# Kernel tuning notes

Measured on AMD Instinct MI355X. Metric: run time of the kernel, lower is better.

The kernel has to match this reference:

```python
import jax, jax.numpy as jnp
import numpy as np

T, M, D_IN, N = 4096, 512, 11, 51


def setup_inputs() -> dict:
    key = jax.random.key(0)
    ks = jax.random.split(key, 11)
    s = 1.0 / np.sqrt(N)  # torch LSTMCell/Linear default init scale
    return {
        "input": jax.random.normal(ks[0], (T, M, D_IN), dtype=jnp.float32),
        "W_ih1": jax.random.uniform(ks[1], (4 * N, D_IN), jnp.float32, -s, s),
        "W_hh1": jax.random.uniform(ks[2], (4 * N, N), jnp.float32, -s, s),
        "b_ih1": jax.random.uniform(ks[3], (4 * N,), jnp.float32, -s, s),
        "b_hh1": jax.random.uniform(ks[4], (4 * N,), jnp.float32, -s, s),
        "W_ih2": jax.random.uniform(ks[5], (4 * N, N), jnp.float32, -s, s),
        "W_hh2": jax.random.uniform(ks[6], (4 * N, N), jnp.float32, -s, s),
        "b_ih2": jax.random.uniform(ks[7], (4 * N,), jnp.float32, -s, s),
        "b_hh2": jax.random.uniform(ks[8], (4 * N,), jnp.float32, -s, s),
        "W_lin": jax.random.uniform(ks[9], (1, N), jnp.float32, -s, s),
        "b_lin": jax.random.uniform(ks[10], (1,), jnp.float32, -s, s),
        "future": 0,
    }


def _lstm_cell(x, h, c, W_ih, W_hh, b_ih, b_hh):
    # torch gate order: input, forget, cell(g), output
    gates = x @ W_ih.T + b_ih + h @ W_hh.T + b_hh  # [m, 4n]
    i, f, g, o = jnp.split(gates, 4, axis=-1)
    c_new = jax.nn.sigmoid(f) * c + jax.nn.sigmoid(i) * jnp.tanh(g)
    h_new = jax.nn.sigmoid(o) * jnp.tanh(c_new)
    return h_new, c_new


def reference(input, W_ih1, W_hh1, b_ih1, b_hh1, W_ih2, W_hh2, b_ih2, b_hh2,
              W_lin, b_lin, future):
    m = input.shape[1]
    n = W_hh1.shape[1]
    h1 = jnp.zeros((m, n), jnp.float32)
    c1 = jnp.zeros((m, n), jnp.float32)
    h2 = jnp.zeros((m, n), jnp.float32)
    c2 = jnp.zeros((m, n), jnp.float32)

    def step(carry, x_t):
        h1, c1, h2, c2 = carry
        h1, c1 = _lstm_cell(x_t, h1, c1, W_ih1, W_hh1, b_ih1, b_hh1)
        h2, c2 = _lstm_cell(h1, h2, c2, W_ih2, W_hh2, b_ih2, b_hh2)
        out = h2 @ W_lin.T + b_lin  # [m, 1]
        return (h1, c1, h2, c2), out

    _, outs = jax.lax.scan(step, (h1, c1, h2, c2), input)  # [T, m, 1]
    # torch.stack(outputs, 1).squeeze(2) -> [m, T]
    # (future loop is dimensionally invalid in the original for future>0; future=0)
    return outs[:, :, 0].T
```

## Files before the change

kernel.cpp:

```cpp
#include <hip/hip_runtime.h>

#define T_STEPS 4096
#define M_BATCH 512
#define D_INP   11
#define N_HID   51
#define L1S     76
#define L2S     140

typedef __attribute__((ext_vector_type(8))) short bf16x8;
typedef __attribute__((ext_vector_type(4))) float f32x4;
typedef __attribute__((ext_vector_type(4))) short s16x4;

__device__ __forceinline__ float sigmoid_fast(float v) {
    return __builtin_amdgcn_rcpf(1.0f + __expf(-v));
}
__device__ __forceinline__ float tanh_fast(float v) {
    return 2.0f * __builtin_amdgcn_rcpf(1.0f + __expf(-2.0f * v)) - 1.0f;
}
__device__ __forceinline__ ushort f2bf(float f) {
    uint u = __float_as_uint(f);
    u += 0x7fffu + ((u >> 16) & 1u);
    return (ushort)(u >> 16);
}
__device__ __forceinline__ float bf2f(ushort h) {
    return __uint_as_float(((uint)h) << 16);
}

#define MFMA(A,B,C) __builtin_amdgcn_mfma_f32_16x16x32_bf16((A),(B),(C),0,0,0)

__attribute__((amdgpu_waves_per_eu(2, 2)))
__global__ __launch_bounds__(512)
void lstm2_mfma8(const float* __restrict__ input,
                 const float* __restrict__ W_ih1, const float* __restrict__ W_hh1,
                 const float* __restrict__ b_ih1, const float* __restrict__ b_hh1,
                 const float* __restrict__ W_ih2, const float* __restrict__ W_hh2,
                 const float* __restrict__ b_ih2, const float* __restrict__ b_hh2,
                 const float* __restrict__ W_lin, const float* __restrict__ b_lin,
                 float* __restrict__ out)
{
    const int tid  = threadIdx.x;
    const int wid  = tid >> 6;
    const int lane = tid & 63;
    const int mr   = lane & 15;
    const int g    = lane >> 4;
    const int col0 = blockIdx.x * 16;
    const bool isL1 = wid < 3;
    const int  m0   = isL1 ? ((wid == 0) ? 0 : (wid == 1) ? 5 : 10)
                           : (wid - 3) * 3;

    __shared__ __align__(16) ushort l1act[16][L1S];
    __shared__ __align__(16) ushort l2act[16][L2S];
    __shared__ __align__(16) ushort xck[2][16][16][12];
    __shared__ __align__(16) float  outb[16][64];

    for (int i = tid; i < 16 * L1S; i += 512) (&l1act[0][0])[i] = 0;
    for (int i = tid; i < 16 * L2S; i += 512) (&l2act[0][0])[i] = 0;
    for (int i = tid; i < 2 * 16 * 16 * 12; i += 512) (&xck[0][0][0][0])[i] = 0;
    for (int i = tid; i < 16 * 64; i += 512) (&outb[0][0])[i] = 0.f;

    float xr[6];
    auto xissue = [&](int cn) {
        #pragma unroll
        for (int i = 0; i < 6; ++i) {
            int f = i * 512 + tid;
            if (f < 2816) {
                int s = f / 176, r2 = f - s * 176;
                int cc = r2 / 11, d = r2 - cc * 11;
                int ts = cn * 16 + s; if (ts > T_STEPS - 1) ts = T_STEPS - 1;
                xr[i] = input[((size_t)ts * M_BATCH + col0 + cc) * D_INP + d];
            }
        }
    };
    auto xwrite = [&](int cn) {
        #pragma unroll
        for (int i = 0; i < 6; ++i) {
            int f = i * 512 + tid;
            if (f < 2816) {
                int s = f / 176, r2 = f - s * 176;
                int cc = r2 / 11, d = r2 - cc * 11;
                xck[cn & 1][s][cc][d] = f2bf(xr[i]);
            }
        }
    };

    auto wgetL1 = [&](int r, int k) -> float {
        if (r >= 204) return 0.f;
        int u = r >> 2, q = r & 3;
        if (k < 12) return (k < 11) ? W_ih1[(q * 51 + u) * 11 + k] : 0.f;
        int hu = k - 12; return (hu < 51) ? W_hh1[(q * 51 + u) * 51 + hu] : 0.f;
    };
    auto wgetL2 = [&](int r, int k) -> float {
        if (r == 204) return (k >= 51 && k < 102) ? W_lin[k - 51] : 0.f;
        if (r > 204) return 0.f;
        int u = r >> 2, q = r & 3;
        if (k < 51)  return W_ih2[(q * 51 + u) * 51 + k];
        if (k < 102) return W_hh2[(q * 51 + u) * 51 + (k - 51)];
        return 0.f;
    };
    auto mkfragL1 = [&](int m, int kt, int ver) -> bf16x8 {
        bf16x8 fr;
        #pragma unroll
        for (int j = 0; j < 8; ++j) {
            int k = 32 * kt + 16 * (j >> 2) + 4 * g + (j & 3);
            float w = wgetL1(16 * m + mr, k);
            ushort hi = f2bf(w);
            fr[j] = (short)((ver == 0) ? hi : f2bf(w - bf2f(hi)));
        }
        return fr;
    };
    auto mkfragL2 = [&](int m, int kt, int ver) -> bf16x8 {
        bf16x8 fr;
        #pragma unroll
        for (int j = 0; j < 8; ++j) {
            int k = 32 * kt + 16 * (j >> 2) + 4 * g + (j & 3);
            float w = wgetL2(16 * m + mr, k);
            ushort hi = f2bf(w);
            fr[j] = (short)((ver == 0) ? hi : f2bf(w - bf2f(hi)));
        }
        return fr;
    };

    bf16x8 afr[24];
    if (wid < 2) {
        #pragma unroll
        for (int mt = 0; mt < 5; ++mt)
            #pragma unroll
            for (int kt = 0; kt < 2; ++kt)
                #pragma unroll
                for (int v = 0; v < 2; ++v)
                    afr[(mt * 2 + kt) * 2 + v] = mkfragL1(m0 + mt, kt, v);
    } else if (wid == 2) {
        #pragma unroll
        for (int mt = 0; mt < 3; ++mt)
            #pragma unroll
            for (int kt = 0; kt < 2; ++kt)
                #pragma unroll
                for (int v = 0; v < 2; ++v)
                    afr[(mt * 2 + kt) * 2 + v] = mkfragL1(m0 + mt, kt, v);
    } else if (wid < 7) {
        #pragma unroll
        for (int mt = 0; mt < 3; ++mt)
            #pragma unroll
            for (int kt = 0; kt < 4; ++kt)
                #pragma unroll
                for (int v = 0; v < 2; ++v)
                    afr[(mt * 4 + kt) * 2 + v] = mkfragL2(m0 + mt, kt, v);
    } else {
        #pragma unroll
        for (int kt = 0; kt < 4; ++kt)
            #pragma unroll
            for (int v = 0; v < 2; ++v)
                afr[kt * 2 + v] = mkfragL2(12, kt, v);
    }

    f32x4 br[5];
    #pragma unroll
    for (int mt = 0; mt < 5; ++mt) {
        int u = 4 * (m0 + mt) + g;
        f32x4 b = {0.f, 0.f, 0.f, 0.f};
        if (u < N_HID) {
            #pragma unroll
            for (int q = 0; q < 4; ++q)
                b[q] = isL1 ? (b_ih1[q * 51 + u] + b_hh1[q * 51 + u])
                            : (b_ih2[q * 51 + u] + b_hh2[q * 51 + u]);
        } else if (!isL1 && u == N_HID) {
            b[0] = b_lin[0];
        }
        br[mt] = b;
    }

    f32x4 acc[5];
    float cst[5];
    #pragma unroll
    for (int i = 0; i < 5; ++i) cst[i] = 0.f;

    auto lstm = [&](f32x4 gg, float& cs) -> float {
        float iv = sigmoid_fast(gg.x), fv = sigmoid_fast(gg.y);
        float gv = tanh_fast(gg.z),    ov = sigmoid_fast(gg.w);
        cs = fv * cs + iv * gv;
        return ov * tanh_fast(cs);
    };

    xissue(0); xwrite(0);
    __syncthreads();

    #pragma unroll 1
    for (int t = 0; t <= T_STEPS + 1; ++t) {
        const int xb = (t >> 4) & 1, xs = t & 15;

        if ((t & 15) == 2 && t <= T_STEPS - 14) xissue((t >> 4) + 1);

        auto loadB1 = [&](int kt) -> bf16x8 {
            int k0 = 32 * kt + 4 * g;
            const ushort* pa = (k0 < 12) ? &xck[xb][xs][mr][k0] : &l1act[mr][k0 - 12];
            s16x4 va = *(const s16x4*)pa;
            s16x4 vb = *(const s16x4*)&l1act[mr][k0 + 4];
            bf16x8 r;
            r[0]=va[0]; r[1]=va[1]; r[2]=va[2]; r[3]=va[3];
            r[4]=vb[0]; r[5]=vb[1]; r[6]=vb[2]; r[7]=vb[3];
            return r;
        };
        auto loadB2 = [&](int kt) -> bf16x8 {
            int k0 = 32 * kt + 4 * g;
            s16x4 va = *(const s16x4*)&l2act[mr][k0];
            s16x4 vb = *(const s16x4*)&l2act[mr][k0 + 16];
            bf16x8 r;
            r[0]=va[0]; r[1]=va[1]; r[2]=va[2]; r[3]=va[3];
            r[4]=vb[0]; r[5]=vb[1]; r[6]=vb[2]; r[7]=vb[3];
            return r;
        };

        if (isL1) {
            bf16x8 b0 = loadB1(0), b1 = loadB1(1);
            if (wid < 2) {
                #pragma unroll
                for (int mt = 0; mt < 5; ++mt) {
                    f32x4 aH = {0.f,0.f,0.f,0.f}, aL = {0.f,0.f,0.f,0.f};
                    aH = MFMA(afr[(mt*2+0)*2+0], b0, aH);
                    aH = MFMA(afr[(mt*2+1)*2+0], b1, aH);
                    aL = MFMA(afr[(mt*2+0)*2+1], b0, aL);
                    aL = MFMA(afr[(mt*2+1)*2+1], b1, aL);
                    acc[mt] = aH + aL;
                }
            } else {
                #pragma unroll
                for (int mt = 0; mt < 3; ++mt) {
                    f32x4 aH = {0.f,0.f,0.f,0.f}, aL = {0.f,0.f,0.f,0.f};
                    aH = MFMA(afr[(mt*2+0)*2+0], b0, aH);
                    aH = MFMA(afr[(mt*2+1)*2+0], b1, aH);
                    aL = MFMA(afr[(mt*2+0)*2+1], b0, aL);
                    aL = MFMA(afr[(mt*2+1)*2+1], b1, aL);
                    acc[mt] = aH + aL;
                }
            }
        } else {
            bf16x8 c0 = loadB2(0), c1 = loadB2(1), c2 = loadB2(2), c3 = loadB2(3);
            if (wid < 7) {
                #pragma unroll
                for (int mt = 0; mt < 3; ++mt) {
                    f32x4 aH = {0.f,0.f,0.f,0.f}, aL = {0.f,0.f,0.f,0.f};
                    aH = MFMA(afr[(mt*4+0)*2+0], c0, aH);
                    aH = MFMA(afr[(mt*4+1)*2+0], c1, aH);
                    aH = MFMA(afr[(mt*4+2)*2+0], c2, aH);
                    aH = MFMA(afr[(mt*4+3)*2+0], c3, aH);
                    aL = MFMA(afr[(mt*4+0)*2+1], c0, aL);
                    aL = MFMA(afr[(mt*4+1)*2+1], c1, aL);
                    aL = MFMA(afr[(mt*4+2)*2+1], c2, aL);
                    aL = MFMA(afr[(mt*4+3)*2+1], c3, aL);
                    acc[mt] = aH + aL;
                }
            } else {
                f32x4 aH = {0.f,0.f,0.f,0.f}, aL = {0.f,0.f,0.f,0.f};
                aH = MFMA(afr[0*2+0], c0, aH);
                aH = MFMA(afr[1*2+0], c1, aH);
                aH = MFMA(afr[2*2+0], c2, aH);
                aH = MFMA(afr[3*2+0], c3, aH);
                aL = MFMA(afr[0*2+1], c0, aL);
                aL = MFMA(afr[1*2+1], c1, aL);
                aL = MFMA(afr[2*2+1], c2, aL);
                aL = MFMA(afr[3*2+1], c3, aL);
                acc[0] = aH + aL;
            }
        }
        __syncthreads();

        if (wid < 2) {
            #pragma unroll
            for (int mt = 0; mt < 5; ++mt) {
                f32x4 gg = acc[mt] + br[mt];
                float h = lstm(gg, cst[mt]);
                int u = 4 * (m0 + mt) + g;
                ushort hb = f2bf(h);
                l1act[mr][u] = hb; l2act[mr][u] = hb;
            }
        } else if (wid == 2) {
            #pragma unroll
            for (int mt = 0; mt < 3; ++mt) {
                f32x4 gg = acc[mt] + br[mt];
                float h = lstm(gg, cst[mt]);
                int u = 4 * (10 + mt) + g;
                if (u < N_HID) { ushort hb = f2bf(h); l1act[mr][u] = hb; l2act[mr][u] = hb; }
            }
        } else if (wid < 7) {
            if (t >= 1) {
                #pragma unroll
                for (int mt = 0; mt < 3; ++mt) {
                    f32x4 gg = acc[mt] + br[mt];
                    float h = lstm(gg, cst[mt]);
                    int u = 4 * (m0 + mt) + g;
                    l2act[mr][N_HID + u] = f2bf(h);
                }
            }
        } else {
            f32x4 gg = acc[0] + br[0];
            if (g == 3) {
                if (t >= 2) outb[mr][(t - 2) & 63] = gg.x;
            } else if (t >= 1) {
                float h = lstm(gg, cst[0]);
                l2act[mr][N_HID + 48 + g] = f2bf(h);
            }
        }

        if ((t & 15) == 10 && t <= T_STEPS - 6) xwrite((t >> 4) + 1);

        if ((t & 31) == 2 && t >= 34) {
            int tb0 = t - 34, cc = tid >> 5, j = tid & 31;
            out[(size_t)(col0 + cc) * T_STEPS + tb0 + j] = outb[cc][(tb0 + j) & 63];
        }
        __syncthreads();
    }

    {
        int tb0 = 4064, cc = tid >> 5, j = tid & 31;
        out[(size_t)(col0 + cc) * T_STEPS + tb0 + j] = outb[cc][(tb0 + j) & 63];
    }
}

extern "C" void kernel_launch(void* const* d_in, const int* in_sizes, int n_in,
                              void* d_out, int out_size, void* d_ws, size_t ws_size,
                              hipStream_t stream) {
    const float* input = (const float*)d_in[0];
    const float* W_ih1 = (const float*)d_in[1];
    const float* W_hh1 = (const float*)d_in[2];
    const float* b_ih1 = (const float*)d_in[3];
    const float* b_hh1 = (const float*)d_in[4];
    const float* W_ih2 = (const float*)d_in[5];
    const float* W_hh2 = (const float*)d_in[6];
    const float* b_ih2 = (const float*)d_in[7];
    const float* b_hh2 = (const float*)d_in[8];
    const float* W_lin = (const float*)d_in[9];
    const float* b_lin = (const float*)d_in[10];
    float* out = (float*)d_out;

    lstm2_mfma8<<<M_BATCH / 16, 512, 0, stream>>>(
        input, W_ih1, W_hh1, b_ih1, b_hh1,
        W_ih2, W_hh2, b_ih2, b_hh2, W_lin, b_lin, out);
}
```

Measured before the change: 5.058 ms.

## Spread LSTM gate tiles over 16 waves with double-buffered activations

Doubles the workgroup to 1024 threads (16 waves, 8 per layer) so each wave handles at most two 16-row gate tiles instead of up to five, shortening the per-step critical path. Hidden-state buffers are merged and double-buffered by timestep parity, which removes the mid-step barrier so only one __syncthreads per step remains. The linear-output wave is folded into the last layer-2 wave. The cost is more waves competing for the CU, fewer registers per wave, and a heavier block-wide barrier.

```diff
diff --git a/kernel.cpp b/kernel.cpp
--- a/kernel.cpp
+++ b/kernel.cpp
@@ -4,8 +4,7 @@
 #define M_BATCH 512
 #define D_INP   11
 #define N_HID   51
-#define L1S     76
-#define L2S     140
+#define ACTS    140
 
 typedef __attribute__((ext_vector_type(8))) short bf16x8;
 typedef __attribute__((ext_vector_type(4))) float f32x4;
@@ -28,15 +27,15 @@
 
 #define MFMA(A,B,C) __builtin_amdgcn_mfma_f32_16x16x32_bf16((A),(B),(C),0,0,0)
 
-__attribute__((amdgpu_waves_per_eu(2, 2)))
-__global__ __launch_bounds__(512)
-void lstm2_mfma8(const float* __restrict__ input,
-                 const float* __restrict__ W_ih1, const float* __restrict__ W_hh1,
-                 const float* __restrict__ b_ih1, const float* __restrict__ b_hh1,
-                 const float* __restrict__ W_ih2, const float* __restrict__ W_hh2,
-                 const float* __restrict__ b_ih2, const float* __restrict__ b_hh2,
-                 const float* __restrict__ W_lin, const float* __restrict__ b_lin,
-                 float* __restrict__ out)
+__attribute__((amdgpu_waves_per_eu(4, 4)))
+__global__ __launch_bounds__(1024)
+void lstm2_mfma16(const float* __restrict__ input,
+                  const float* __restrict__ W_ih1, const float* __restrict__ W_hh1,
+                  const float* __restrict__ b_ih1, const float* __restrict__ b_hh1,
+                  const float* __restrict__ W_ih2, const float* __restrict__ W_hh2,
+                  const float* __restrict__ b_ih2, const float* __restrict__ b_hh2,
+                  const float* __restrict__ W_lin, const float* __restrict__ b_lin,
+                  float* __restrict__ out)
 {
     const int tid  = threadIdx.x;
     const int wid  = tid >> 6;
@@ -44,25 +43,23 @@
     const int mr   = lane & 15;
     const int g    = lane >> 4;
     const int col0 = blockIdx.x * 16;
-    const bool isL1 = wid < 3;
-    const int  m0   = isL1 ? ((wid == 0) ? 0 : (wid == 1) ? 5 : 10)
-                           : (wid - 3) * 3;
-
-    __shared__ __align__(16) ushort l1act[16][L1S];
-    __shared__ __align__(16) ushort l2act[16][L2S];
+    const bool isL1 = wid < 8;
+    const int  lw   = isL1 ? wid : wid - 8;
+    const int  m0   = (lw < 5) ? lw * 2 : 10 + (lw - 5);
+
+    __shared__ __align__(16) ushort act[2][16][ACTS];
     __shared__ __align__(16) ushort xck[2][16][16][12];
     __shared__ __align__(16) float  outb[16][64];
 
-    for (int i = tid; i < 16 * L1S; i += 512) (&l1act[0][0])[i] = 0;
-    for (int i = tid; i < 16 * L2S; i += 512) (&l2act[0][0])[i] = 0;
-    for (int i = tid; i < 2 * 16 * 16 * 12; i += 512) (&xck[0][0][0][0])[i] = 0;
-    for (int i = tid; i < 16 * 64; i += 512) (&outb[0][0])[i] = 0.f;
-
-    float xr[6];
+    for (int i = tid; i < 2 * 16 * ACTS; i += 1024) (&act[0][0][0])[i] = 0;
+    for (int i = tid; i < 2 * 16 * 16 * 12; i += 1024) (&xck[0][0][0][0])[i] = 0;
+    for (int i = tid; i < 16 * 64; i += 1024) (&outb[0][0])[i] = 0.f;
+
+    float xr[3];
     auto xissue = [&](int cn) {
         #pragma unroll
-        for (int i = 0; i < 6; ++i) {
-            int f = i * 512 + tid;
+        for (int i = 0; i < 3; ++i) {
+            int f = i * 1024 + tid;
             if (f < 2816) {
                 int s = f / 176, r2 = f - s * 176;
                 int cc = r2 / 11, d = r2 - cc * 11;
@@ -73,8 +70,8 @@
     };
     auto xwrite = [&](int cn) {
         #pragma unroll
-        for (int i = 0; i < 6; ++i) {
-            int f = i * 512 + tid;
+        for (int i = 0; i < 3; ++i) {
+            int f = i * 1024 + tid;
             if (f < 2816) {
                 int s = f / 176, r2 = f - s * 176;
                 int cc = r2 / 11, d = r2 - cc * 11;
@@ -120,42 +117,44 @@
         return fr;
     };
 
-    bf16x8 afr[24];
-    if (wid < 2) {
-        #pragma unroll
-        for (int mt = 0; mt < 5; ++mt)
+    bf16x8 afr[16];
+    if (isL1) {
+        if (lw < 5) {
+            #pragma unroll
+            for (int mt = 0; mt < 2; ++mt)
+                #pragma unroll
+                for (int kt = 0; kt < 2; ++kt)
+                    #pragma unroll
+                    for (int v = 0; v < 2; ++v)
+                        afr[(mt * 2 + kt) * 2 + v] = mkfragL1(m0 + mt, kt, v);
+        } else {
             #pragma unroll
             for (int kt = 0; kt < 2; ++kt)
                 #pragma unroll
                 for (int v = 0; v < 2; ++v)
-                    afr[(mt * 2 + kt) * 2 + v] = mkfragL1(m0 + mt, kt, v);
-    } else if (wid == 2) {
-        #pragma unroll
-        for (int mt = 0; mt < 3; ++mt)
-            #pragma unroll
-            for (int kt = 0; kt < 2; ++kt)
+                    afr[kt * 2 + v] = mkfragL1(m0, kt, v);
+        }
+    } else {
+        if (lw < 5) {
+            #pragma unroll
+            for (int mt = 0; mt < 2; ++mt)
+                #pragma unroll
+                for (int kt = 0; kt < 4; ++kt)
+                    #pragma unroll
+                    for (int v = 0; v < 2; ++v)
+                        afr[(mt * 4 + kt) * 2 + v] = mkfragL2(m0 + mt, kt, v);
+        } else {
+            #pragma unroll
+            for (int kt = 0; kt < 4; ++kt)
                 #pragma unroll
                 for (int v = 0; v < 2; ++v)
-                    afr[(mt * 2 + kt) * 2 + v] = mkfragL1(m0 + mt, kt, v);
-    } else if (wid < 7) {
-        #pragma unroll
-        for (int mt = 0; mt < 3; ++mt)
-            #pragma unroll
-            for (int kt = 0; kt < 4; ++kt)
-                #pragma unroll
-                for (int v = 0; v < 2; ++v)
-                    afr[(mt * 4 + kt) * 2 + v] = mkfragL2(m0 + mt, kt, v);
-    } else {
-        #pragma unroll
-        for (int kt = 0; kt < 4; ++kt)
-            #pragma unroll
-            for (int v = 0; v < 2; ++v)
-                afr[kt * 2 + v] = mkfragL2(12, kt, v);
+                    afr[kt * 2 + v] = mkfragL2(m0, kt, v);
+        }
     }
 
-    f32x4 br[5];
+    f32x4 br[2];
     #pragma unroll
-    for (int mt = 0; mt < 5; ++mt) {
+    for (int mt = 0; mt < 2; ++mt) {
         int u = 4 * (m0 + mt) + g;
         f32x4 b = {0.f, 0.f, 0.f, 0.f};
         if (u < N_HID) {
@@ -169,10 +168,8 @@
         br[mt] = b;
     }
 
-    f32x4 acc[5];
-    float cst[5];
-    #pragma unroll
-    for (int i = 0; i < 5; ++i) cst[i] = 0.f;
+    f32x4 acc[2];
+    float cst[2] = {0.f, 0.f};
 
     auto lstm = [&](f32x4 gg, float& cs) -> float {
         float iv = sigmoid_fast(gg.x), fv = sigmoid_fast(gg.y);
@@ -181,20 +178,23 @@
         return ov * tanh_fast(cs);
     };
 
-    xissue(0); xwrite(0);
+    xissue(0);
+    __syncthreads();
+    xwrite(0);
     __syncthreads();
 
     #pragma unroll 1
     for (int t = 0; t <= T_STEPS + 1; ++t) {
-        const int xb = (t >> 4) & 1, xs = t & 15;
+        const int p = t & 1, q = p ^ 1;
+        const int xb = (t >> 4) & 1, xst = t & 15;
 
         if ((t & 15) == 2 && t <= T_STEPS - 14) xissue((t >> 4) + 1);
 
         auto loadB1 = [&](int kt) -> bf16x8 {
             int k0 = 32 * kt + 4 * g;
-            const ushort* pa = (k0 < 12) ? &xck[xb][xs][mr][k0] : &l1act[mr][k0 - 12];
+            const ushort* pa = (k0 < 12) ? &xck[xb][xst][mr][k0] : &act[p][mr][k0 - 12];
             s16x4 va = *(const s16x4*)pa;
-            s16x4 vb = *(const s16x4*)&l1act[mr][k0 + 4];
+            s16x4 vb = *(const s16x4*)&act[p][mr][k0 + 4];
             bf16x8 r;
             r[0]=va[0]; r[1]=va[1]; r[2]=va[2]; r[3]=va[3];
             r[4]=vb[0]; r[5]=vb[1]; r[6]=vb[2]; r[7]=vb[3];
@@ -202,8 +202,8 @@
         };
         auto loadB2 = [&](int kt) -> bf16x8 {
             int k0 = 32 * kt + 4 * g;
-            s16x4 va = *(const s16x4*)&l2act[mr][k0];
-            s16x4 vb = *(const s16x4*)&l2act[mr][k0 + 16];
+            s16x4 va = *(const s16x4*)&act[p][mr][k0];
+            s16x4 vb = *(const s16x4*)&act[p][mr][k0 + 16];
             bf16x8 r;
             r[0]=va[0]; r[1]=va[1]; r[2]=va[2]; r[3]=va[3];
             r[4]=vb[0]; r[5]=vb[1]; r[6]=vb[2]; r[7]=vb[3];
@@ -212,9 +212,9 @@
 
         if (isL1) {
             bf16x8 b0 = loadB1(0), b1 = loadB1(1);
-            if (wid < 2) {
-                #pragma unroll
-                for (int mt = 0; mt < 5; ++mt) {
+            if (lw < 5) {
+                #pragma unroll
+                for (int mt = 0; mt < 2; ++mt) {
                     f32x4 aH = {0.f,0.f,0.f,0.f}, aL = {0.f,0.f,0.f,0.f};
                     aH = MFMA(afr[(mt*2+0)*2+0], b0, aH);
                     aH = MFMA(afr[(mt*2+1)*2+0], b1, aH);
@@ -223,21 +223,18 @@
                     acc[mt] = aH + aL;
                 }
             } else {
-                #pragma unroll
-                for (int mt = 0; mt < 3; ++mt) {
-                    f32x4 aH = {0.f,0.f,0.f,0.f}, aL = {0.f,0.f,0.f,0.f};
-                    aH = MFMA(afr[(mt*2+0)*2+0], b0, aH);
-                    aH = MFMA(afr[(mt*2+1)*2+0], b1, aH);
-                    aL = MFMA(afr[(mt*2+0)*2+1], b0, aL);
-                    aL = MFMA(afr[(mt*2+1)*2+1], b1, aL);
-                    acc[mt] = aH + aL;
-                }
+                f32x4 aH = {0.f,0.f,0.f,0.f}, aL = {0.f,0.f,0.f,0.f};
+                aH = MFMA(afr[0*2+0], b0, aH);
+                aH = MFMA(afr[1*2+0], b1, aH);
+                aL = MFMA(afr[0*2+1], b0, aL);
+                aL = MFMA(afr[1*2+1], b1, aL);
+                acc[0] = aH + aL;
             }
         } else {
             bf16x8 c0 = loadB2(0), c1 = loadB2(1), c2 = loadB2(2), c3 = loadB2(3);
-            if (wid < 7) {
-                #pragma unroll
-                for (int mt = 0; mt < 3; ++mt) {
+            if (lw < 5) {
+                #pragma unroll
+                for (int mt = 0; mt < 2; ++mt) {
                     f32x4 aH = {0.f,0.f,0.f,0.f}, aL = {0.f,0.f,0.f,0.f};
                     aH = MFMA(afr[(mt*4+0)*2+0], c0, aH);
                     aH = MFMA(afr[(mt*4+1)*2+0], c1, aH);
@@ -262,57 +259,57 @@
                 acc[0] = aH + aL;
             }
         }
-        __syncthreads();
-
-        if (wid < 2) {
-            #pragma unroll
-            for (int mt = 0; mt < 5; ++mt) {
-                f32x4 gg = acc[mt] + br[mt];
-                float h = lstm(gg, cst[mt]);
-                int u = 4 * (m0 + mt) + g;
-                ushort hb = f2bf(h);
-                l1act[mr][u] = hb; l2act[mr][u] = hb;
-            }
-        } else if (wid == 2) {
-            #pragma unroll
-            for (int mt = 0; mt < 3; ++mt) {
-                f32x4 gg = acc[mt] + br[mt];
-                float h = lstm(gg, cst[mt]);
-                int u = 4 * (10 + mt) + g;
-                if (u < N_HID) { ushort hb = f2bf(h); l1act[mr][u] = hb; l2act[mr][u] = hb; }
-            }
-        } else if (wid < 7) {
-            if (t >= 1) {
-                #pragma unroll
-                for (int mt = 0; mt < 3; ++mt) {
+
+        if (isL1) {
+            if (lw < 5) {
+                #pragma unroll
+                for (int mt = 0; mt < 2; ++mt) {
                     f32x4 gg = acc[mt] + br[mt];
                     float h = lstm(gg, cst[mt]);
-                    int u = 4 * (m0 + mt) + g;
-                    l2act[mr][N_HID + u] = f2bf(h);
+                    act[q][mr][4 * (m0 + mt) + g] = f2bf(h);
                 }
+            } else {
+                int u = 4 * m0 + g;
+                f32x4 gg = acc[0] + br[0];
+                float h = lstm(gg, cst[0]);
+                if (u < N_HID) act[q][mr][u] = f2bf(h);
             }
         } else {
-            f32x4 gg = acc[0] + br[0];
-            if (g == 3) {
-                if (t >= 2) outb[mr][(t - 2) & 63] = gg.x;
-            } else if (t >= 1) {
-                float h = lstm(gg, cst[0]);
-                l2act[mr][N_HID + 48 + g] = f2bf(h);
+            if (t >= 1) {
+                if (lw < 5) {
+                    #pragma unroll
+                    for (int mt = 0; mt < 2; ++mt) {
+                        f32x4 gg = acc[mt] + br[mt];
+                        float h = lstm(gg, cst[mt]);
+                        act[q][mr][N_HID + 4 * (m0 + mt) + g] = f2bf(h);
+                    }
+                } else {
+                    int u = 4 * m0 + g;
+                    f32x4 gg = acc[0] + br[0];
+                    if (u < N_HID) {
+                        float h = lstm(gg, cst[0]);
+                        act[q][mr][N_HID + u] = f2bf(h);
+                    } else if (u == N_HID && t >= 2) {
+                        outb[mr][(t - 2) & 63] = gg.x;
+                    }
+                }
             }
         }
 
         if ((t & 15) == 10 && t <= T_STEPS - 6) xwrite((t >> 4) + 1);
 
-        if ((t & 31) == 2 && t >= 34) {
-            int tb0 = t - 34, cc = tid >> 5, j = tid & 31;
-            out[(size_t)(col0 + cc) * T_STEPS + tb0 + j] = outb[cc][(tb0 + j) & 63];
+        if ((t & 31) == 2 && t >= 34 && tid < 512) {
+            int cc = tid >> 5, s = tid & 31;
+            int tb = t - 35 + s;
+            if (tb >= 0) out[(size_t)(col0 + cc) * T_STEPS + tb] = outb[cc][tb & 63];
         }
         __syncthreads();
     }
 
-    {
-        int tb0 = 4064, cc = tid >> 5, j = tid & 31;
-        out[(size_t)(col0 + cc) * T_STEPS + tb0 + j] = outb[cc][(tb0 + j) & 63];
+    if (tid < 528) {
+        int cc = tid / 33, s = tid - cc * 33;
+        int tb = 4063 + s;
+        out[(size_t)(col0 + cc) * T_STEPS + tb] = outb[cc][tb & 63];
     }
 }
 
@@ -332,7 +329,7 @@
     const float* b_lin = (const float*)d_in[10];
     float* out = (float*)d_out;
 
-    lstm2_mfma8<<<M_BATCH / 16, 512, 0, stream>>>(
+    lstm2_mfma16<<<M_BATCH / 16, 1024, 0, stream>>>(
         input, W_ih1, W_hh1, b_ih1, b_hh1,
         W_ih2, W_hh2, b_ih2, b_hh2, W_lin, b_lin, out);
 }
```

Result: slower. 5.959 ms (+17.8%).
